# Performance work log

Hardware: AMD Instinct MI355X
Metric: run time of the kernel (lower is better)

Reference implementation:

```python
import jax, jax.numpy as jnp
import numpy as np

K = 15  # dynamic kernel size (out conv emits 15*15=225 channels)


def conv3x3(x, w, b):
    # x: [B,C,H,W], w: [O,I,3,3] (OIHW), 'SAME' padding, stride 1
    y = jax.lax.conv_general_dilated(
        x, w, window_strides=(1, 1), padding='SAME',
        dimension_numbers=('NCHW', 'OIHW', 'NCHW'))
    return y + b[None, :, None, None]


def res_block(x, wa, ba, wb, bb):
    # ResidualBlock_noBN: x + conv(relu(conv(x)))
    return x + conv3x3(jax.nn.relu(conv3x3(x, wa, ba)), wb, bb)


def setup_inputs() -> dict:
    key = jax.random.key(0)
    ks = jax.random.split(key, 12)
    nf = 64

    def w(k, o, i):
        return jax.random.normal(k, (o, i, 3, 3), jnp.float32) * 0.05

    return {
        'data_with_est': jax.random.normal(ks[0], (4, 6, 256, 256), jnp.float32),
        'data': jax.random.normal(ks[1], (4, 3, 256, 256), jnp.float32),
        'w_first': w(ks[2], nf, 6), 'b_first': jnp.zeros((nf,), jnp.float32),
        'w1a': w(ks[3], nf, nf), 'b1a': jnp.zeros((nf,), jnp.float32),
        'w1b': w(ks[4], nf, nf), 'b1b': jnp.zeros((nf,), jnp.float32),
        'w2a': w(ks[5], nf, nf), 'b2a': jnp.zeros((nf,), jnp.float32),
        'w2b': w(ks[6], nf, nf), 'b2b': jnp.zeros((nf,), jnp.float32),
        'w3a': w(ks[7], nf, nf), 'b3a': jnp.zeros((nf,), jnp.float32),
        'w3b': w(ks[8], nf, nf), 'b3b': jnp.zeros((nf,), jnp.float32),
        'w_out': w(ks[9], K * K, nf), 'b_out': jnp.zeros((K * K,), jnp.float32),
    }


def kernel_conv(frames, core):
    # frames: [B,3,H,W]; core: [B,225,H,W]
    B, C, H, W = frames.shape
    # per-pixel softmax over the 225 kernel taps of |core| (N=1, color=1 in original view)
    weights = jax.nn.softmax(jnp.abs(core), axis=1)  # [B, K*K, H, W]
    p = K // 2
    pad = jnp.pad(frames, ((0, 0), (0, 0), (p, p), (p, p)))
    shifts = jnp.arange(K)

    def win(i, j):  # shifted window, matches frame_pad[..., i:i+H, j:j+W]
        return jax.lax.dynamic_slice(pad, (0, 0, i, j), (B, C, H, W))

    # [K, K, B, C, H, W]; flattened index i*K+j matches torch stacking order
    patches = jax.vmap(lambda i: jax.vmap(lambda j: win(i, j))(shifts))(shifts)
    patches = patches.reshape(K * K, B, C, H, W)
    pred = jnp.einsum('bkhw,kbchw->bchw', weights, patches)  # sum over taps
    return pred


def reference(data_with_est, data,
              w_first, b_first,
              w1a, b1a, w1b, b1b,
              w2a, b2a, w2b, b2b,
              w3a, b3a, w3b, b3b,
              w_out, b_out):
    x = conv3x3(data_with_est, w_first, b_first)
    x = res_block(x, w1a, b1a, w1b, b1b)
    x = res_block(x, w2a, b2a, w2b, b2b)
    x = res_block(x, w3a, b3a, w3b, b3b)
    core = conv3x3(x, w_out, b_out)  # [B,225,H,W]
    pred = kernel_conv(data, core)   # [B,3,H,W]
    # original returns [frames, pred]
    return (data, pred)
```

## Files before the change

### kernel.cpp

```cpp
#include <hip/hip_runtime.h>

#define HW 256
#define PW 258
#define PP (PW * PW)
#define NPIX (HW * HW)

using short8 = __attribute__((ext_vector_type(8))) short;
using short4v = __attribute__((ext_vector_type(4))) short;
using f32x4 = __attribute__((ext_vector_type(4))) float;
using h4 = __attribute__((ext_vector_type(4))) _Float16;
using h8 = __attribute__((ext_vector_type(8))) _Float16;

#define GLD_LDS(g, l)                                                  \
  __builtin_amdgcn_global_load_lds(                                    \
      (const __attribute__((address_space(1))) void*)(g),              \
      (__attribute__((address_space(3))) void*)(l), 16, 0, 0)

static __device__ __forceinline__ ushort f2bf(float f) {
  unsigned u = __float_as_uint(f);
  unsigned r = (u + 0x7FFFu + ((u >> 16) & 1u)) >> 16;
  return (ushort)r;
}
static __device__ __forceinline__ float bf2f(ushort u) {
  return __uint_as_float(((unsigned)u) << 16);
}

__global__ void pack_in_k(const float* __restrict__ din, ushort* __restrict__ xp) {
  int i = blockIdx.x * 256 + threadIdx.x;
  int b = i >> 16;
  int px = i & 65535;
  int y = px >> 8, x = px & 255;
  short8 v;
#pragma unroll
  for (int z = 0; z < 8; ++z) v[z] = 0;
#pragma unroll
  for (int ic = 0; ic < 6; ++ic)
    v[ic] = (short)f2bf(din[(b * 6 + ic) * NPIX + px]);
  *(short8*)&xp[((size_t)b * PP + (size_t)(y + 1) * PW + (x + 1)) * 8] = v;
}

__global__ void zero_halo_k(ushort* __restrict__ x, ushort* __restrict__ y,
                            ushort* __restrict__ xp) {
  int i = blockIdx.x * 256 + threadIdx.x;
  if (i >= 4 * 1028) return;
  int b = i / 1028;
  int h = i - b * 1028;
  int py, px;
  if (h < 258) { py = 0; px = h; }
  else if (h < 516) { py = 257; px = h - 258; }
  else if (h < 772) { py = h - 516 + 1; px = 0; }
  else { py = h - 772 + 1; px = 257; }
  size_t p = (size_t)b * PP + (size_t)py * PW + px;
  short8 z;
#pragma unroll
  for (int k = 0; k < 8; ++k) z[k] = 0;
#pragma unroll
  for (int c8 = 0; c8 < 8; ++c8) {
    *(short8*)&x[p * 64 + c8 * 8] = z;
    *(short8*)&y[p * 64 + c8 * 8] = z;
  }
  *(short8*)&xp[p * 8] = z;
}

__global__ void pack_wfrag_k(const float* __restrict__ w,
                             ushort* __restrict__ wf, int OC, int CIN,
                             int CPAD, int NG, int total) {
  int i = blockIdx.x * 256 + threadIdx.x;
  if (i >= total) return;
  int j = i & 7;
  int lane = (i >> 3) & 63;
  int rest = i >> 9;
  int g = rest % NG;
  int ks = rest / NG;
  int oc = g * 16 + (lane & 15);
  int k = ks * 32 + (lane >> 4) * 8 + j;
  int t = k / CPAD;
  int ic = k - t * CPAD;
  float v = 0.f;
  if (oc < OC && t < 9 && ic < CIN) v = w[(oc * CIN + ic) * 9 + t];
  wf[i] = f2bf(v);
}

template <int C, int KS, bool RELU, bool RESID>
__global__ __launch_bounds__(256, 2) void conv_mfma_k(
    const ushort* __restrict__ in, const ushort* __restrict__ wf,
    const float* __restrict__ bias, const ushort* __restrict__ resid,
    ushort* __restrict__ out) {
  constexpr int CV = C / 8;
  constexpr int SROW = 66 * CV;
  constexpr int TOT = 6 * SROW;
  constexpr int LSLOT = ((TOT + 63) / 64) * 64;
  constexpr int NCH = KS / 3;
  constexpr int NBUF = (NCH > 1) ? 2 : 1;
  constexpr int CHW = 3 * 4 * 64 * 8;
  __shared__ __align__(16) ushort wLds[NBUF * CHW];
  __shared__ __align__(16) ushort xs[LSLOT * 8];

  const int tid = threadIdx.x;
  const int wave = tid >> 6, lane = tid & 63;
  const int quad = lane >> 4, l15 = lane & 15;
  const int x0 = blockIdx.x * 64, y0 = blockIdx.y * 4, b = blockIdx.z;
  const ushort* inb = in + (size_t)b * PP * C;

  for (int s0 = wave * 64; s0 < TOT; s0 += 256) {
    int s = s0 + lane;
    int row, col, chunk;
    if (C == 64) {
      row = s / SROW;
      int r = s - row * SROW;
      col = r >> 3;
      chunk = (r & 7) ^ (col & 7);
    } else {
      row = s / 66;
      col = s - row * 66;
      chunk = 0;
    }
    GLD_LDS(inb + ((size_t)(y0 + row) * PW + (x0 + col)) * C + chunk * 8,
            &xs[(size_t)s0 * 8]);
  }
#pragma unroll
  for (int r = 0; r < 3; ++r) {
    int s0 = r * 256 + wave * 64;
    GLD_LDS(wf + (size_t)(s0 + lane) * 8, &wLds[s0 * 8]);
  }
  __syncthreads();

  f32x4 acc[4][4];
#pragma unroll
  for (int mt = 0; mt < 4; ++mt)
#pragma unroll
    for (int nt = 0; nt < 4; ++nt)
#pragma unroll
      for (int r = 0; r < 4; ++r) acc[mt][nt][r] = 0.f;

#pragma unroll
  for (int ch = 0; ch < NCH; ++ch) {
    if (ch + 1 < NCH) {
      const ushort* src = wf + (size_t)(ch + 1) * CHW;
      ushort* dst = &wLds[((ch + 1) % NBUF) * CHW];
#pragma unroll
      for (int r = 0; r < 3; ++r) {
        int s0 = r * 256 + wave * 64;
        GLD_LDS(src + (size_t)(s0 + lane) * 8, dst + s0 * 8);
      }
    }
    const ushort* wb = &wLds[(ch % NBUF) * CHW];
#pragma unroll
    for (int ksl = 0; ksl < 3; ++ksl) {
      const int ks = ch * 3 + ksl;
      short8 A[4], B[4];
#pragma unroll
      for (int mt = 0; mt < 4; ++mt)
        A[mt] = *(const short8*)&wb[((ksl * 4 + mt) * 64 + lane) * 8];
      int t, chunk;
      if (C == 64) {
        t = ks >> 1;
        chunk = ((ks & 1) << 2) + quad;
      } else {
        t = ks * 4 + quad;
        if (t > 8) t = 8;
        chunk = 0;
      }
      int dy = t / 3, dx = t - (t / 3) * 3;
#pragma unroll
      for (int nt = 0; nt < 4; ++nt) {
        int c = nt * 16 + l15 + dx;
        int slot = (C == 64)
                       ? ((wave + dy) * SROW + c * 8 + (chunk ^ (c & 7)))
                       : ((wave + dy) * 66 + c);
        B[nt] = *(const short8*)&xs[(size_t)slot * 8];
      }
#pragma unroll
      for (int nt = 0; nt < 4; ++nt)
#pragma unroll
        for (int mt = 0; mt < 4; ++mt)
          acc[mt][nt] = __builtin_amdgcn_mfma_f32_16x16x32_bf16(
              A[mt], B[nt], acc[mt][nt], 0, 0, 0);
    }
    if (NCH > 1) __syncthreads();
  }

  const int yw = y0 + wave;
#pragma unroll
  for (int mt = 0; mt < 4; ++mt) {
    const float4 bb = *(const float4*)&bias[mt * 16 + quad * 4];
#pragma unroll
    for (int nt = 0; nt < 4; ++nt) {
      int px = x0 + nt * 16 + l15;
      size_t base = ((size_t)b * PP + (size_t)(yw + 1) * PW + (px + 1)) * 64 +
                    mt * 16 + quad * 4;
      float v0 = acc[mt][nt][0] + bb.x;
      float v1 = acc[mt][nt][1] + bb.y;
      float v2 = acc[mt][nt][2] + bb.z;
      float v3 = acc[mt][nt][3] + bb.w;
      if (RELU) {
        v0 = fmaxf(v0, 0.f); v1 = fmaxf(v1, 0.f);
        v2 = fmaxf(v2, 0.f); v3 = fmaxf(v3, 0.f);
      }
      if (RESID) {
        short4v rv = *(const short4v*)&resid[base];
        v0 += bf2f((ushort)rv[0]); v1 += bf2f((ushort)rv[1]);
        v2 += bf2f((ushort)rv[2]); v3 += bf2f((ushort)rv[3]);
      }
      short4v o;
      o[0] = (short)f2bf(v0); o[1] = (short)f2bf(v1);
      o[2] = (short)f2bf(v2); o[3] = (short)f2bf(v3);
      *(short4v*)&out[base] = o;
    }
  }
}

__global__ __launch_bounds__(256, 2) void out_kc_k(
    const ushort* __restrict__ x, const ushort* __restrict__ wf,
    const float* __restrict__ b_out, const float* __restrict__ data,
    float* __restrict__ pred) {
  constexpr int CHW = 16 * 64 * 8;
  __shared__ __align__(16) char uni[2 * CHW * 2 + 1600 * 16];
  __shared__ float dsh[3][15][78];
  __shared__ float bsh[256];
  ushort* wLds = (ushort*)uni;
  ushort* xs = (ushort*)(uni + 2 * CHW * 2);
  _Float16* coreSh = (_Float16*)uni;

  const int tid = threadIdx.x;
  const int wave = tid >> 6, lane = tid & 63;
  const int quad = lane >> 4, l15 = lane & 15;
  const int x0 = blockIdx.x * 64, y = blockIdx.y, b = blockIdx.z;

  for (int s0 = wave * 64; s0 < 3 * 528; s0 += 256) {
    int s = s0 + lane;
    int row = s / 528;
    int r = s - row * 528;
    int col = r >> 3;
    int chunk = (r & 7) ^ (col & 7);
    const ushort* g = x + ((size_t)b * PP + (size_t)(y + row) * PW +
                           (x0 + col)) * 64 + chunk * 8;
    GLD_LDS(g, &xs[(size_t)s0 * 8]);
  }
#pragma unroll
  for (int r = 0; r < 4; ++r) {
    int s0 = r * 256 + wave * 64;
    GLD_LDS(wf + (size_t)(s0 + lane) * 8, &wLds[s0 * 8]);
  }
  bsh[tid] = (tid < 225) ? b_out[tid] : 0.f;
  for (int i = tid; i < 3 * 15 * 78; i += 256) {
    int ch = i / 1170;
    int rem = i - ch * 1170;
    int r = rem / 78;
    int cc = rem - r * 78;
    int gy = y - 7 + r, gx = x0 - 7 + cc;
    float v = 0.f;
    if ((unsigned)gy < (unsigned)HW && (unsigned)gx < (unsigned)HW)
      v = data[((b * 3 + ch) << 16) + (gy << 8) + gx];
    dsh[ch][r][cc] = v;
  }
  __syncthreads();

  f32x4 acc[4][4];
#pragma unroll
  for (int mt = 0; mt < 4; ++mt)
#pragma unroll
    for (int nt = 0; nt < 4; ++nt)
#pragma unroll
      for (int r = 0; r < 4; ++r) acc[mt][nt][r] = 0.f;

#pragma unroll
  for (int ks = 0; ks < 18; ++ks) {
    if (ks + 1 < 18) {
      const ushort* src = wf + (size_t)(ks + 1) * CHW;
      ushort* dst = &wLds[((ks + 1) & 1) * CHW];
#pragma unroll
      for (int r = 0; r < 4; ++r) {
        int s0 = r * 256 + wave * 64;
        GLD_LDS(src + (size_t)(s0 + lane) * 8, dst + s0 * 8);
      }
    }
    const ushort* wb = &wLds[(ks & 1) * CHW];
    short8 A[4], B[4];
#pragma unroll
    for (int mt = 0; mt < 4; ++mt)
      A[mt] = *(const short8*)&wb[((wave * 4 + mt) * 64 + lane) * 8];
    int t = ks >> 1;
    int dy = t / 3, dx = t - (t / 3) * 3;
    int chunk = ((ks & 1) << 2) + quad;
#pragma unroll
    for (int nt = 0; nt < 4; ++nt) {
      int c = nt * 16 + l15 + dx;
      int slot = dy * 528 + c * 8 + (chunk ^ (c & 7));
      B[nt] = *(const short8*)&xs[(size_t)slot * 8];
    }
#pragma unroll
    for (int nt = 0; nt < 4; ++nt)
#pragma unroll
      for (int mt = 0; mt < 4; ++mt)
        acc[mt][nt] = __builtin_amdgcn_mfma_f32_16x16x32_bf16(
            A[mt], B[nt], acc[mt][nt], 0, 0, 0);
    __syncthreads();
  }

#pragma unroll
  for (int mt = 0; mt < 4; ++mt) {
    int c0 = wave * 64 + mt * 16 + quad * 4;
#pragma unroll
    for (int nt = 0; nt < 4; ++nt) {
      int px = nt * 16 + l15;
      h4 hv;
#pragma unroll
      for (int r = 0; r < 4; ++r) {
        int c = c0 + r;
        float a = acc[mt][nt][r] + bsh[c];
        a = (c < 225) ? fabsf(a) : -1e4f;
        hv[r] = (_Float16)a;
      }
      *(h4*)&coreSh[px * 264 + c0] = hv;
    }
  }
  __syncthreads();

  const int px = wave * 16 + l15;
  const int cbase = quad * 64;
  h8 vals[8];
#pragma unroll
  for (int v = 0; v < 8; ++v)
    vals[v] = *(h8*)&coreSh[px * 264 + cbase + v * 8];

  float m = 0.f;
#pragma unroll
  for (int v = 0; v < 8; ++v)
#pragma unroll
    for (int z = 0; z < 8; ++z) m = fmaxf(m, (float)vals[v][z]);
  m = fmaxf(m, __shfl_xor(m, 16));
  m = fmaxf(m, __shfl_xor(m, 32));

  float l = 0.f, p0 = 0.f, p1 = 0.f, p2 = 0.f;
#pragma unroll
  for (int v = 0; v < 8; ++v)
#pragma unroll
    for (int z = 0; z < 8; ++z) {
      int c = cbase + v * 8 + z;
      float a = (float)vals[v][z];
      float e = __expf(a - m);
      l += e;
      if (c < 225) {
        int di = (int)(((unsigned)c * 34953u) >> 19);
        int dj = c - di * 15;
        p0 += e * dsh[0][di][px + dj];
        p1 += e * dsh[1][di][px + dj];
        p2 += e * dsh[2][di][px + dj];
      }
    }
  l += __shfl_xor(l, 16);  l += __shfl_xor(l, 32);
  p0 += __shfl_xor(p0, 16); p0 += __shfl_xor(p0, 32);
  p1 += __shfl_xor(p1, 16); p1 += __shfl_xor(p1, 32);
  p2 += __shfl_xor(p2, 16); p2 += __shfl_xor(p2, 32);

  if (quad == 0) {
    float inv = 1.f / l;
    int pix = (y << 8) + x0 + px;
    pred[((b * 3 + 0) << 16) + pix] = p0 * inv;
    pred[((b * 3 + 1) << 16) + pix] = p1 * inv;
    pred[((b * 3 + 2) << 16) + pix] = p2 * inv;
  }
}

__global__ void copy_k(const float4* __restrict__ src, float4* __restrict__ dst,
                       int n4) {
  int i = blockIdx.x * blockDim.x + threadIdx.x;
  if (i < n4) dst[i] = src[i];
}

extern "C" void kernel_launch(void* const* d_in, const int* in_sizes, int n_in,
                              void* d_out, int out_size, void* d_ws,
                              size_t ws_size, hipStream_t stream) {
  const float* data_with_est = (const float*)d_in[0];
  const float* data = (const float*)d_in[1];
  const float* w_first = (const float*)d_in[2];
  const float* b_first = (const float*)d_in[3];
  const float* wa[3] = {(const float*)d_in[4], (const float*)d_in[8],
                        (const float*)d_in[12]};
  const float* ba[3] = {(const float*)d_in[5], (const float*)d_in[9],
                        (const float*)d_in[13]};
  const float* wb[3] = {(const float*)d_in[6], (const float*)d_in[10],
                        (const float*)d_in[14]};
  const float* bb[3] = {(const float*)d_in[7], (const float*)d_in[11],
                        (const float*)d_in[15]};
  const float* w_out = (const float*)d_in[16];
  const float* b_out = (const float*)d_in[17];

  float* out = (float*)d_out;
  float* pred = out + 4 * 3 * NPIX;

  ushort* x = (ushort*)d_ws;
  ushort* y = x + (size_t)4 * PP * 64;
  ushort* xp = y + (size_t)4 * PP * 64;
  ushort* Wp1 = xp + (size_t)4 * PP * 8;
  ushort* Wpr = Wp1 + 6144;
  ushort* Wpo = Wpr + 6 * 36864;

  pack_in_k<<<1024, 256, 0, stream>>>(data_with_est, xp);
  zero_halo_k<<<17, 256, 0, stream>>>(x, y, xp);
  pack_wfrag_k<<<24, 256, 0, stream>>>(w_first, Wp1, 64, 6, 8, 4, 6144);
  for (int i = 0; i < 3; ++i) {
    pack_wfrag_k<<<144, 256, 0, stream>>>(wa[i], Wpr + (2 * i) * 36864, 64, 64,
                                          64, 4, 36864);
    pack_wfrag_k<<<144, 256, 0, stream>>>(wb[i], Wpr + (2 * i + 1) * 36864, 64,
                                          64, 64, 4, 36864);
  }
  pack_wfrag_k<<<576, 256, 0, stream>>>(w_out, Wpo, 225, 64, 64, 16, 147456);

  dim3 cgrid(4, 64, 4), cblk(256);
  conv_mfma_k<8, 3, false, false>
      <<<cgrid, cblk, 0, stream>>>(xp, Wp1, b_first, nullptr, x);
  for (int i = 0; i < 3; ++i) {
    conv_mfma_k<64, 18, true, false><<<cgrid, cblk, 0, stream>>>(
        x, Wpr + (2 * i) * 36864, ba[i], nullptr, y);
    conv_mfma_k<64, 18, false, true><<<cgrid, cblk, 0, stream>>>(
        y, Wpr + (2 * i + 1) * 36864, bb[i], x, x);
  }
  out_kc_k<<<dim3(4, HW, 4), 256, 0, stream>>>(x, Wpo, b_out, data, pred);
  int n4 = 4 * 3 * NPIX / 4;
  copy_k<<<(n4 + 255) / 256, 256, 0, stream>>>((const float4*)data,
                                               (float4*)out, n4);
}
```

Measured before the change: 500.2 us.

## Load conv input fragments directly from global memory instead of LDS staging

Removes the LDS staging of the input halo tile in both the residual conv kernel and the fused output/kernel-conv kernel. MFMA B operands are now read straight from global memory (relying on L1/L2 for reuse across taps). The freed LDS raises the occupancy target to 3 blocks per SM, and the core scratch row stride changes from 264 to 280. The cost is repeated global/cache traffic for each tap and more load latency on the MFMA critical path.

```diff
diff --git a/kernel.cpp b/kernel.cpp
--- a/kernel.cpp
+++ b/kernel.cpp
@@ -82,19 +82,14 @@
 }
 
 template <int C, int KS, bool RELU, bool RESID>
-__global__ __launch_bounds__(256, 2) void conv_mfma_k(
+__global__ __launch_bounds__(256, 3) void conv_mfma_k(
     const ushort* __restrict__ in, const ushort* __restrict__ wf,
     const float* __restrict__ bias, const ushort* __restrict__ resid,
     ushort* __restrict__ out) {
-  constexpr int CV = C / 8;
-  constexpr int SROW = 66 * CV;
-  constexpr int TOT = 6 * SROW;
-  constexpr int LSLOT = ((TOT + 63) / 64) * 64;
   constexpr int NCH = KS / 3;
   constexpr int NBUF = (NCH > 1) ? 2 : 1;
   constexpr int CHW = 3 * 4 * 64 * 8;
   __shared__ __align__(16) ushort wLds[NBUF * CHW];
-  __shared__ __align__(16) ushort xs[LSLOT * 8];
 
   const int tid = threadIdx.x;
   const int wave = tid >> 6, lane = tid & 63;
@@ -102,22 +97,6 @@
   const int x0 = blockIdx.x * 64, y0 = blockIdx.y * 4, b = blockIdx.z;
   const ushort* inb = in + (size_t)b * PP * C;
 
-  for (int s0 = wave * 64; s0 < TOT; s0 += 256) {
-    int s = s0 + lane;
-    int row, col, chunk;
-    if (C == 64) {
-      row = s / SROW;
-      int r = s - row * SROW;
-      col = r >> 3;
-      chunk = (r & 7) ^ (col & 7);
-    } else {
-      row = s / 66;
-      col = s - row * 66;
-      chunk = 0;
-    }
-    GLD_LDS(inb + ((size_t)(y0 + row) * PW + (x0 + col)) * C + chunk * 8,
-            &xs[(size_t)s0 * 8]);
-  }
 #pragma unroll
   for (int r = 0; r < 3; ++r) {
     int s0 = r * 256 + wave * 64;
@@ -164,11 +143,10 @@
       int dy = t / 3, dx = t - (t / 3) * 3;
 #pragma unroll
       for (int nt = 0; nt < 4; ++nt) {
-        int c = nt * 16 + l15 + dx;
-        int slot = (C == 64)
-                       ? ((wave + dy) * SROW + c * 8 + (chunk ^ (c & 7)))
-                       : ((wave + dy) * 66 + c);
-        B[nt] = *(const short8*)&xs[(size_t)slot * 8];
+        const ushort* gp =
+            inb + ((size_t)(y0 + wave + dy) * PW + (x0 + nt * 16 + l15 + dx)) *
+                      C + chunk * 8;
+        B[nt] = *(const short8*)gp;
       }
 #pragma unroll
       for (int nt = 0; nt < 4; ++nt)
@@ -210,16 +188,15 @@
   }
 }
 
-__global__ __launch_bounds__(256, 2) void out_kc_k(
+__global__ __launch_bounds__(256, 3) void out_kc_k(
     const ushort* __restrict__ x, const ushort* __restrict__ wf,
     const float* __restrict__ b_out, const float* __restrict__ data,
     float* __restrict__ pred) {
   constexpr int CHW = 16 * 64 * 8;
-  __shared__ __align__(16) char uni[2 * CHW * 2 + 1600 * 16];
+  __shared__ __align__(16) char uni[64 * 280 * 2];
   __shared__ float dsh[3][15][78];
   __shared__ float bsh[256];
   ushort* wLds = (ushort*)uni;
-  ushort* xs = (ushort*)(uni + 2 * CHW * 2);
   _Float16* coreSh = (_Float16*)uni;
 
   const int tid = threadIdx.x;
@@ -227,16 +204,6 @@
   const int quad = lane >> 4, l15 = lane & 15;
   const int x0 = blockIdx.x * 64, y = blockIdx.y, b = blockIdx.z;
 
-  for (int s0 = wave * 64; s0 < 3 * 528; s0 += 256) {
-    int s = s0 + lane;
-    int row = s / 528;
-    int r = s - row * 528;
-    int col = r >> 3;
-    int chunk = (r & 7) ^ (col & 7);
-    const ushort* g = x + ((size_t)b * PP + (size_t)(y + row) * PW +
-                           (x0 + col)) * 64 + chunk * 8;
-    GLD_LDS(g, &xs[(size_t)s0 * 8]);
-  }
 #pragma unroll
   for (int r = 0; r < 4; ++r) {
     int s0 = r * 256 + wave * 64;
@@ -285,9 +252,9 @@
     int chunk = ((ks & 1) << 2) + quad;
 #pragma unroll
     for (int nt = 0; nt < 4; ++nt) {
-      int c = nt * 16 + l15 + dx;
-      int slot = dy * 528 + c * 8 + (chunk ^ (c & 7));
-      B[nt] = *(const short8*)&xs[(size_t)slot * 8];
+      const ushort* gp = x + ((size_t)b * PP + (size_t)(y + dy) * PW +
+                              (x0 + nt * 16 + l15 + dx)) * 64 + chunk * 8;
+      B[nt] = *(const short8*)gp;
     }
 #pragma unroll
     for (int nt = 0; nt < 4; ++nt)
@@ -312,7 +279,7 @@
         a = (c < 225) ? fabsf(a) : -1e4f;
         hv[r] = (_Float16)a;
       }
-      *(h4*)&coreSh[px * 264 + c0] = hv;
+      *(h4*)&coreSh[px * 280 + c0] = hv;
     }
   }
   __syncthreads();
@@ -322,7 +289,7 @@
   h8 vals[8];
 #pragma unroll
   for (int v = 0; v < 8; ++v)
-    vals[v] = *(h8*)&coreSh[px * 264 + cbase + v * 8];
+    vals[v] = *(h8*)&coreSh[px * 280 + cbase + v * 8];
 
   float m = 0.f;
 #pragma unroll
```

Measured after the change: 692.5 us. 1.38x slower.

## Stream conv weights from global into registers instead of LDS double-buffering

Applied to the files above, without the earlier changes.

Both the trunk conv kernel and the fused output conv/kernel-prediction kernel stop staging weight fragments in LDS. Instead, each lane loads its A fragments directly from global memory (L2-cached) into a register ring of six k-steps, prefetched ahead of use. B fragments from the input tile are software-pipelined one step ahead in registers. This removes the per-chunk LDS weight copies and the __syncthreads barriers in the main loop and shrinks LDS usage. The cost is much higher VGPR pressure, which could cause spills or reduced occupancy, and global-load latency now sits directly in the MFMA loop.

```diff
diff --git a/kernel.cpp b/kernel.cpp
--- a/kernel.cpp
+++ b/kernel.cpp
@@ -90,10 +90,7 @@
   constexpr int SROW = 66 * CV;
   constexpr int TOT = 6 * SROW;
   constexpr int LSLOT = ((TOT + 63) / 64) * 64;
-  constexpr int NCH = KS / 3;
-  constexpr int NBUF = (NCH > 1) ? 2 : 1;
-  constexpr int CHW = 3 * 4 * 64 * 8;
-  __shared__ __align__(16) ushort wLds[NBUF * CHW];
+  constexpr int W = (KS > 6) ? 6 : KS;
   __shared__ __align__(16) ushort xs[LSLOT * 8];
 
   const int tid = threadIdx.x;
@@ -101,6 +98,7 @@
   const int quad = lane >> 4, l15 = lane & 15;
   const int x0 = blockIdx.x * 64, y0 = blockIdx.y * 4, b = blockIdx.z;
   const ushort* inb = in + (size_t)b * PP * C;
+  const ushort* wfl = wf + (size_t)lane * 8;
 
   for (int s0 = wave * 64; s0 < TOT; s0 += 256) {
     int s = s0 + lane;
@@ -118,11 +116,16 @@
     GLD_LDS(inb + ((size_t)(y0 + row) * PW + (x0 + col)) * C + chunk * 8,
             &xs[(size_t)s0 * 8]);
   }
-#pragma unroll
-  for (int r = 0; r < 3; ++r) {
-    int s0 = r * 256 + wave * 64;
-    GLD_LDS(wf + (size_t)(s0 + lane) * 8, &wLds[s0 * 8]);
-  }
+
+  short8 Wa[4][W];
+  auto loadA = [&](int slot, int ks) {
+#pragma unroll
+    for (int mt = 0; mt < 4; ++mt)
+      Wa[mt][slot] = *(const short8*)&wfl[(size_t)(ks * 4 + mt) * 512];
+  };
+#pragma unroll
+  for (int ks = 0; ks < W; ++ks) loadA(ks, ks);
+
   __syncthreads();
 
   f32x4 acc[4][4];
@@ -133,51 +136,42 @@
 #pragma unroll
       for (int r = 0; r < 4; ++r) acc[mt][nt][r] = 0.f;
 
-#pragma unroll
-  for (int ch = 0; ch < NCH; ++ch) {
-    if (ch + 1 < NCH) {
-      const ushort* src = wf + (size_t)(ch + 1) * CHW;
-      ushort* dst = &wLds[((ch + 1) % NBUF) * CHW];
-#pragma unroll
-      for (int r = 0; r < 3; ++r) {
-        int s0 = r * 256 + wave * 64;
-        GLD_LDS(src + (size_t)(s0 + lane) * 8, dst + s0 * 8);
-      }
-    }
-    const ushort* wb = &wLds[(ch % NBUF) * CHW];
-#pragma unroll
-    for (int ksl = 0; ksl < 3; ++ksl) {
-      const int ks = ch * 3 + ksl;
-      short8 A[4], B[4];
+  auto loadB = [&](short8* B, int ks) {
+    int t, chunk;
+    if (C == 64) {
+      t = ks >> 1;
+      chunk = ((ks & 1) << 2) + quad;
+    } else {
+      t = ks * 4 + quad;
+      if (t > 8) t = 8;
+      chunk = 0;
+    }
+    int dy = t / 3, dx = t - (t / 3) * 3;
+#pragma unroll
+    for (int nt = 0; nt < 4; ++nt) {
+      int c = nt * 16 + l15 + dx;
+      int slot = (C == 64)
+                     ? ((wave + dy) * SROW + c * 8 + (chunk ^ (c & 7)))
+                     : ((wave + dy) * 66 + c);
+      B[nt] = *(const short8*)&xs[(size_t)slot * 8];
+    }
+  };
+
+  short8 B0[4], B1[4];
+  loadB(B0, 0);
+#pragma unroll
+  for (int ks = 0; ks < KS; ++ks) {
+    if (ks + 1 < KS) loadB(B1, ks + 1);
+    const int slot = ks % W;
+#pragma unroll
+    for (int nt = 0; nt < 4; ++nt)
 #pragma unroll
       for (int mt = 0; mt < 4; ++mt)
-        A[mt] = *(const short8*)&wb[((ksl * 4 + mt) * 64 + lane) * 8];
-      int t, chunk;
-      if (C == 64) {
-        t = ks >> 1;
-        chunk = ((ks & 1) << 2) + quad;
-      } else {
-        t = ks * 4 + quad;
-        if (t > 8) t = 8;
-        chunk = 0;
-      }
-      int dy = t / 3, dx = t - (t / 3) * 3;
-#pragma unroll
-      for (int nt = 0; nt < 4; ++nt) {
-        int c = nt * 16 + l15 + dx;
-        int slot = (C == 64)
-                       ? ((wave + dy) * SROW + c * 8 + (chunk ^ (c & 7)))
-                       : ((wave + dy) * 66 + c);
-        B[nt] = *(const short8*)&xs[(size_t)slot * 8];
-      }
-#pragma unroll
-      for (int nt = 0; nt < 4; ++nt)
-#pragma unroll
-        for (int mt = 0; mt < 4; ++mt)
-          acc[mt][nt] = __builtin_amdgcn_mfma_f32_16x16x32_bf16(
-              A[mt], B[nt], acc[mt][nt], 0, 0, 0);
-    }
-    if (NCH > 1) __syncthreads();
+        acc[mt][nt] = __builtin_amdgcn_mfma_f32_16x16x32_bf16(
+            Wa[mt][slot], B0[nt], acc[mt][nt], 0, 0, 0);
+    if (ks + W < KS) loadA(slot, ks + W);
+#pragma unroll
+    for (int nt = 0; nt < 4; ++nt) B0[nt] = B1[nt];
   }
 
   const int yw = y0 + wave;
@@ -214,18 +208,17 @@
     const ushort* __restrict__ x, const ushort* __restrict__ wf,
     const float* __restrict__ b_out, const float* __restrict__ data,
     float* __restrict__ pred) {
-  constexpr int CHW = 16 * 64 * 8;
-  __shared__ __align__(16) char uni[2 * CHW * 2 + 1600 * 16];
+  __shared__ __align__(16) char uni[64 * 264 * 2];
   __shared__ float dsh[3][15][78];
   __shared__ float bsh[256];
-  ushort* wLds = (ushort*)uni;
-  ushort* xs = (ushort*)(uni + 2 * CHW * 2);
+  ushort* xs = (ushort*)uni;
   _Float16* coreSh = (_Float16*)uni;
 
   const int tid = threadIdx.x;
   const int wave = tid >> 6, lane = tid & 63;
   const int quad = lane >> 4, l15 = lane & 15;
   const int x0 = blockIdx.x * 64, y = blockIdx.y, b = blockIdx.z;
+  const ushort* wfl = wf + (size_t)lane * 8;
 
   for (int s0 = wave * 64; s0 < 3 * 528; s0 += 256) {
     int s = s0 + lane;
@@ -236,11 +229,6 @@
     const ushort* g = x + ((size_t)b * PP + (size_t)(y + row) * PW +
                            (x0 + col)) * 64 + chunk * 8;
     GLD_LDS(g, &xs[(size_t)s0 * 8]);
-  }
-#pragma unroll
-  for (int r = 0; r < 4; ++r) {
-    int s0 = r * 256 + wave * 64;
-    GLD_LDS(wf + (size_t)(s0 + lane) * 8, &wLds[s0 * 8]);
   }
   bsh[tid] = (tid < 225) ? b_out[tid] : 0.f;
   for (int i = tid; i < 3 * 15 * 78; i += 256) {
@@ -254,6 +242,17 @@
       v = data[((b * 3 + ch) << 16) + (gy << 8) + gx];
     dsh[ch][r][cc] = v;
   }
+
+  short8 Wa[4][6];
+  auto loadA = [&](int slot, int ks) {
+#pragma unroll
+    for (int mt = 0; mt < 4; ++mt)
+      Wa[mt][slot] =
+          *(const short8*)&wfl[(size_t)((ks * 16 + wave * 4 + mt)) * 512];
+  };
+#pragma unroll
+  for (int ks = 0; ks < 6; ++ks) loadA(ks, ks);
+
   __syncthreads();
 
   f32x4 acc[4][4];
@@ -264,22 +263,7 @@
 #pragma unroll
       for (int r = 0; r < 4; ++r) acc[mt][nt][r] = 0.f;
 
-#pragma unroll
-  for (int ks = 0; ks < 18; ++ks) {
-    if (ks + 1 < 18) {
-      const ushort* src = wf + (size_t)(ks + 1) * CHW;
-      ushort* dst = &wLds[((ks + 1) & 1) * CHW];
-#pragma unroll
-      for (int r = 0; r < 4; ++r) {
-        int s0 = r * 256 + wave * 64;
-        GLD_LDS(src + (size_t)(s0 + lane) * 8, dst + s0 * 8);
-      }
-    }
-    const ushort* wb = &wLds[(ks & 1) * CHW];
-    short8 A[4], B[4];
-#pragma unroll
-    for (int mt = 0; mt < 4; ++mt)
-      A[mt] = *(const short8*)&wb[((wave * 4 + mt) * 64 + lane) * 8];
+  auto loadB = [&](short8* B, int ks) {
     int t = ks >> 1;
     int dy = t / 3, dx = t - (t / 3) * 3;
     int chunk = ((ks & 1) << 2) + quad;
@@ -289,14 +273,25 @@
       int slot = dy * 528 + c * 8 + (chunk ^ (c & 7));
       B[nt] = *(const short8*)&xs[(size_t)slot * 8];
     }
+  };
+
+  short8 B0[4], B1[4];
+  loadB(B0, 0);
+#pragma unroll
+  for (int ks = 0; ks < 18; ++ks) {
+    if (ks + 1 < 18) loadB(B1, ks + 1);
+    const int slot = ks % 6;
 #pragma unroll
     for (int nt = 0; nt < 4; ++nt)
 #pragma unroll
       for (int mt = 0; mt < 4; ++mt)
         acc[mt][nt] = __builtin_amdgcn_mfma_f32_16x16x32_bf16(
-            A[mt], B[nt], acc[mt][nt], 0, 0, 0);
-    __syncthreads();
-  }
+            Wa[mt][slot], B0[nt], acc[mt][nt], 0, 0, 0);
+    if (ks + 6 < 18) loadA(slot, ks + 6);
+#pragma unroll
+    for (int nt = 0; nt < 4; ++nt) B0[nt] = B1[nt];
+  }
+  __syncthreads();
 
 #pragma unroll
   for (int mt = 0; mt < 4; ++mt) {
```

Result: faster. 466.8 us (-6.7%).
